# Kernel tuning notes

Measured on AMD Instinct MI355X. Metric: run time of the kernel, lower is better.

Reference implementation:

```python
import jax, jax.numpy as jnp
import numpy as np

B, S, D, H = 4, 1024, 512, 8
EPS = 1e-5


def _cx(x):
    # [..., 2] float -> complex
    return jax.lax.complex(x[..., 0], x[..., 1])


def setup_inputs() -> dict:
    key = jax.random.key(0)
    ks = jax.random.split(key, 9)
    f = lambda k, sh: jax.random.normal(k, sh, dtype=jnp.float32)
    inp = {
        "q": f(ks[0], (B, S, D, 2)),
        "k": f(ks[1], (B, S, D, 2)),
        "v": f(ks[2], (B, S, D, 2)),
        "Wq": f(ks[3], (D, D, 2)) * 0.02,
        "bq": f(ks[4], (D, 2)) * 0.02,
        "Wk": f(ks[5], (D, D, 2)) * 0.02,
        "bk": f(ks[6], (D, 2)) * 0.02,
        "Wv": f(ks[7], (D, D, 2)) * 0.02,
        "bv": f(ks[8], (D, 2)) * 0.02,
        "gamma_r": jnp.ones((D,), jnp.float32),
        "beta_r": jnp.zeros((D,), jnp.float32),
        "gamma_i": jnp.ones((D,), jnp.float32),
        "beta_i": jnp.zeros((D,), jnp.float32),
        "n_heads": H,
    }
    return inp


def _layernorm(x, g, b):
    # torch LayerNorm: biased variance, eps inside sqrt
    mu = jnp.mean(x, axis=-1, keepdims=True)
    var = jnp.mean((x - mu) ** 2, axis=-1, keepdims=True)
    return (x - mu) / jnp.sqrt(var + EPS) * g + b


def reference(q, k, v, Wq, bq, Wk, bk, Wv, bv, gamma_r, beta_r, gamma_i, beta_i, n_heads):
    qc, kc, vc = _cx(q), _cx(k), _cx(v)
    # complex linear: x @ W^T + b
    Q = jnp.einsum("bsd,ed->bse", qc, _cx(Wq)) + _cx(bq)
    K = jnp.einsum("bsd,ed->bse", kc, _cx(Wk)) + _cx(bk)
    V = jnp.einsum("bsd,ed->bse", vc, _cx(Wv)) + _cx(bv)
    b, s, d = qc.shape
    dh = d // n_heads
    Qh = Q.reshape(b, s, n_heads, dh)
    Kh = K.reshape(b, s, n_heads, dh)
    Vh = V.reshape(b, s, n_heads, dh)
    # complex scores [b,h,q,k], scaled by sqrt(dh)
    scores = jnp.einsum("bqhd,bkhd->bhqk", Qh, Kh) / jnp.sqrt(jnp.float32(dh))
    # original: softmax over view_as_real dim=-2 == key axis, real & imag independently
    attn = jax.lax.complex(jax.nn.softmax(scores.real, axis=-1),
                           jax.nn.softmax(scores.imag, axis=-1))
    # (dropout is identity in eval mode)
    out = jnp.einsum("bhqk,bkhd->bqhd", attn, Vh).reshape(b, s, d)
    out = out + qc  # residual
    out_r = _layernorm(out.real, gamma_r, beta_r)
    out_i = _layernorm(out.imag, gamma_i, beta_i)
    return jnp.stack([out_r, out_i], axis=-1)  # [B,S,D,2]
```

## Files before the change

kernel.cpp:

```cpp
#include <hip/hip_runtime.h>
#include <math.h>

#define BB  4
#define SS  1024
#define DD  512
#define HH  8
#define DHD 64
#define PL  2097152
#define WPL 262144

constexpr float LN_EPS = 1e-5f;

using half8 = __attribute__((ext_vector_type(8))) _Float16;
using f32x4 = __attribute__((ext_vector_type(4))) float;

__device__ __forceinline__ half8 negh(half8 a) {
    union { half8 h; unsigned int u[4]; } t;
    t.h = a;
    #pragma unroll
    for (int i = 0; i < 4; ++i) t.u[i] ^= 0x80008000u;
    return t.h;
}
__device__ __forceinline__ half8 ldh64(const unsigned short* p, int row, int col) {
    return *(const half8*)(p + row * 64 + (col ^ ((row & 7) << 3)));
}
__device__ __forceinline__ half8 ldh40(const unsigned short* p, int row, int col) {
    return *(const half8*)(p + row * 40 + col);
}
#define MFMA16(acc, a, b) acc = __builtin_amdgcn_mfma_f32_16x16x32_f16(a, b, acc, 0, 0, 0)

__global__ __launch_bounds__(256)
void cvt_kernel(const float2* __restrict__ s0, const float2* __restrict__ s1,
                const float2* __restrict__ s2, unsigned short* __restrict__ dst,
                int planeElems) {
    const int z = blockIdx.y;
    const float2* src = z == 0 ? s0 : (z == 1 ? s1 : s2);
    unsigned short* base = dst + (size_t)z * 2 * planeElems;
    const int idx = (blockIdx.x * 256 + threadIdx.x) * 2;
    float4 t = *(const float4*)(src + idx);
    union { _Float16 h[2]; unsigned int u; } r, i;
    r.h[0] = (_Float16)t.x; r.h[1] = (_Float16)t.z;
    i.h[0] = (_Float16)t.y; i.h[1] = (_Float16)t.w;
    ((unsigned int*)(base))[idx >> 1] = r.u;
    ((unsigned int*)(base + planeElems))[idx >> 1] = i.u;
}

__global__ __launch_bounds__(256, 5)
void proj_kernel(const unsigned short* __restrict__ XP,
                 const unsigned short* __restrict__ WP,
                 const float2* __restrict__ bq, const float2* __restrict__ bk,
                 const float2* __restrict__ bv,
                 unsigned short* __restrict__ QG, unsigned short* __restrict__ KG,
                 unsigned short* __restrict__ VG) {
    const unsigned short* XR = XP + (size_t)blockIdx.z * 2 * PL;
    const unsigned short* XI = XR + PL;
    const unsigned short* WR = WP + (size_t)blockIdx.z * 2 * WPL;
    const unsigned short* WI = WR + WPL;
    const float2* bias; unsigned short* outP;
    if (blockIdx.z == 0)      { bias = bq; outP = QG; }
    else if (blockIdx.z == 1) { bias = bk; outP = KG; }
    else                      { bias = bv; outP = VG; }
    const bool isV = (blockIdx.z == 2);

    __shared__ unsigned short Xs[2][4096];
    __shared__ unsigned short Ws[2][4096];

    const int tid  = threadIdx.x;
    const int w    = tid >> 6;
    const int lane = tid & 63;
    const int quad = lane >> 4;
    const int l15  = lane & 15;
    const int m0   = blockIdx.x * 64;
    const int h    = blockIdx.y;
    const int e0   = h * 64;

    const int r8 = tid >> 3;
    const int g8 = tid & 7;

    f32x4 Sr[4], Si[4];
    #pragma unroll
    for (int i = 0; i < 4; ++i) { Sr[i] = (f32x4)0.f; Si[i] = (f32x4)0.f; }

    for (int dc = 0; dc < DD; dc += 64) {
        if (dc) __syncthreads();
        #pragma unroll
        for (int it = 0; it < 2; ++it) {
            const int row = it * 32 + r8;
            const int off = row * 64 + ((g8 ^ (row & 7)) << 3);
            const size_t xo = (size_t)(m0 + row) * DD + dc + g8 * 8;
            const size_t wo = (size_t)(e0 + row) * DD + dc + g8 * 8;
            *(uint4*)&Xs[0][off] = *(const uint4*)(XR + xo);
            *(uint4*)&Xs[1][off] = *(const uint4*)(XI + xo);
            *(uint4*)&Ws[0][off] = *(const uint4*)(WR + wo);
            *(uint4*)&Ws[1][off] = *(const uint4*)(WI + wo);
        }
        __syncthreads();

        const int mrow = w * 16 + l15;
        #pragma unroll
        for (int kc = 0; kc < 2; ++kc) {
            const int dl = kc * 32 + quad * 8;
            half8 xr  = ldh64(Xs[0], mrow, dl);
            half8 xi  = ldh64(Xs[1], mrow, dl);
            half8 xmi = negh(xi);
            #pragma unroll
            for (int et = 0; et < 4; ++et) {
                const int er = et * 16 + l15;
                half8 wr = ldh64(Ws[0], er, dl);
                half8 wi = ldh64(Ws[1], er, dl);
                MFMA16(Sr[et], xr,  wr);
                MFMA16(Sr[et], xmi, wi);
                MFMA16(Si[et], xr,  wi);
                MFMA16(Si[et], xi,  wr);
            }
        }
    }

    #pragma unroll
    for (int et = 0; et < 4; ++et) {
        const int col = et * 16 + l15;
        float2 bb = bias[e0 + col];
        #pragma unroll
        for (int reg = 0; reg < 4; ++reg) {
            int m = m0 + w * 16 + quad * 4 + reg;
            int b = m >> 10;
            int s = m & 1023;
            int bh = b * HH + h;
            union { _Float16 h; unsigned short u; } cr, ci;
            cr.h = (_Float16)(Sr[et][reg] + bb.x);
            ci.h = (_Float16)(Si[et][reg] + bb.y);
            size_t o = isV ? ((size_t)bh * DHD + col) * SS + s
                           : ((size_t)bh * SS + s) * DHD + col;
            outP[0 * PL + o] = cr.u;
            outP[1 * PL + o] = ci.u;
        }
    }
}

__global__ __launch_bounds__(256, 3)
void attn_kernel(const unsigned short* __restrict__ QG, const unsigned short* __restrict__ KG,
                 const unsigned short* __restrict__ VG,
                 unsigned short* __restrict__ ObR, unsigned short* __restrict__ ObI) {
    __shared__ unsigned short Ks[2][2048];
    __shared__ unsigned short Vt[2][2560];
    __shared__ unsigned short Ps[2][4][640];

    const int n   = blockIdx.x;
    const int bh  = (n & 7) * 4 + (n >> 7);
    const int q0  = ((n >> 3) & 15) * 64;
    const int b   = bh >> 3;
    const int h   = bh & 7;

    const int tid  = threadIdx.x;
    const int w    = tid >> 6;
    const int lane = tid & 63;
    const int quad = lane >> 4;
    const int l15  = lane & 15;

    half8 qr[2], qi[2], qmi[2];
    #pragma unroll
    for (int kc = 0; kc < 2; ++kc) {
        size_t qb = ((size_t)bh * SS + q0 + w * 16 + l15) * DHD + kc * 32 + quad * 8;
        qr[kc]  = *(const half8*)(QG + 0 * PL + qb);
        qi[kc]  = *(const half8*)(QG + 1 * PL + qb);
        qmi[kc] = negh(qi[kc]);
    }

    f32x4 Arr[4], Ari[4], Air[4], Aii[4];
    #pragma unroll
    for (int i = 0; i < 4; ++i) { Arr[i] = (f32x4)0.f; Ari[i] = (f32x4)0.f; Air[i] = (f32x4)0.f; Aii[i] = (f32x4)0.f; }
    float lrp[4] = {0.f, 0.f, 0.f, 0.f}, lip[4] = {0.f, 0.f, 0.f, 0.f};

    unsigned short* PrW = Ps[0][w];
    unsigned short* PiW = Ps[1][w];

    const int kr = tid >> 3, sg = (tid & 7) * 8;
    const int dv = tid >> 2, sv = (tid & 3) * 8;

    for (int kt = 0; kt < SS; kt += 32) {
        if (kt) __syncthreads();
        #pragma unroll
        for (int p = 0; p < 2; ++p) {
            *(uint4*)&Ks[p][kr * 64 + (sg ^ ((kr & 7) << 3))] =
                *(const uint4*)(KG + (size_t)p * PL + ((size_t)bh * SS + kt + kr) * DHD + sg);
            *(uint4*)&Vt[p][dv * 40 + sv] =
                *(const uint4*)(VG + (size_t)p * PL + ((size_t)bh * DHD + dv) * SS + kt + sv);
        }
        __syncthreads();

        f32x4 Sr[2], Si[2];
        Sr[0] = (f32x4)0.f; Sr[1] = (f32x4)0.f; Si[0] = (f32x4)0.f; Si[1] = (f32x4)0.f;
        #pragma unroll
        for (int kc = 0; kc < 2; ++kc) {
            const int dl = kc * 32 + quad * 8;
            #pragma unroll
            for (int nt = 0; nt < 2; ++nt) {
                const int krow = nt * 16 + l15;
                half8 krF = ldh64(Ks[0], krow, dl);
                half8 kiF = ldh64(Ks[1], krow, dl);
                MFMA16(Sr[nt], qr[kc],  krF);
                MFMA16(Sr[nt], qmi[kc], kiF);
                MFMA16(Si[nt], qr[kc],  kiF);
                MFMA16(Si[nt], qi[kc],  krF);
            }
        }

        #pragma unroll
        for (int nt = 0; nt < 2; ++nt) {
            #pragma unroll
            for (int reg = 0; reg < 4; ++reg) {
                union { _Float16 h; unsigned short u; } cr, ci;
                cr.h = (_Float16)__expf(Sr[nt][reg] * 0.125f);
                ci.h = (_Float16)__expf(Si[nt][reg] * 0.125f);
                lrp[reg] += (float)cr.h;
                lip[reg] += (float)ci.h;
                int qq = quad * 4 + reg;
                int kcol = nt * 16 + l15;
                PrW[qq * 40 + kcol] = cr.u;
                PiW[qq * 40 + kcol] = ci.u;
            }
        }

        {
            const int kl = quad * 8;
            half8 prF = ldh40(PrW, l15, kl);
            half8 piF = ldh40(PiW, l15, kl);
            #pragma unroll
            for (int dt = 0; dt < 4; ++dt) {
                const int d = dt * 16 + l15;
                half8 vrF = ldh40(Vt[0], d, kl);
                half8 viF = ldh40(Vt[1], d, kl);
                MFMA16(Arr[dt], prF, vrF);
                MFMA16(Ari[dt], prF, viF);
                MFMA16(Air[dt], piF, vrF);
                MFMA16(Aii[dt], piF, viF);
            }
        }
    }

    float ir[4], ii[4];
    #pragma unroll
    for (int reg = 0; reg < 4; ++reg) {
        float a = lrp[reg], c = lip[reg];
        #pragma unroll
        for (int mk = 1; mk < 16; mk <<= 1) {
            a += __shfl_xor(a, mk);
            c += __shfl_xor(c, mk);
        }
        ir[reg] = 1.f / a;
        ii[reg] = 1.f / c;
    }
    #pragma unroll
    for (int dt = 0; dt < 4; ++dt) {
        #pragma unroll
        for (int reg = 0; reg < 4; ++reg) {
            int q   = q0 + w * 16 + quad * 4 + reg;
            int col = h * DHD + dt * 16 + l15;
            union { _Float16 h; unsigned short u; } cr, ci;
            cr.h = (_Float16)(Arr[dt][reg] * ir[reg] - Aii[dt][reg] * ii[reg]);
            ci.h = (_Float16)(Ari[dt][reg] * ir[reg] + Air[dt][reg] * ii[reg]);
            size_t o = ((size_t)b * SS + q) * DD + col;
            ObR[o] = cr.u;
            ObI[o] = ci.u;
        }
    }
}

__global__ __launch_bounds__(256)
void ln_kernel(const unsigned short* __restrict__ OrP, const unsigned short* __restrict__ OiP,
               const float2* __restrict__ Qin,
               const float* __restrict__ gr, const float* __restrict__ br,
               const float* __restrict__ gi, const float* __restrict__ bi,
               float2* __restrict__ out) {
    const int row = blockIdx.x;
    const int tid = threadIdx.x;
    const size_t base = (size_t)row * DD;
    const int e0 = 2 * tid, e1 = 2 * tid + 1;

    union { unsigned int u; _Float16 h[2]; } tr, ti;
    tr.u = *(const unsigned int*)(OrP + base + e0);
    ti.u = *(const unsigned int*)(OiP + base + e0);
    float2 r0 = Qin[base + e0];
    float2 r1 = Qin[base + e1];
    float xr0 = (float)tr.h[0] + r0.x;
    float xr1 = (float)tr.h[1] + r1.x;
    float xi0 = (float)ti.h[0] + r0.y;
    float xi1 = (float)ti.h[1] + r1.y;

    float sr = xr0 + xr1;
    float si = xi0 + xi1;
    float qr = xr0 * xr0 + xr1 * xr1;
    float qi = xi0 * xi0 + xi1 * xi1;
    #pragma unroll
    for (int off = 32; off > 0; off >>= 1) {
        sr += __shfl_down(sr, off);
        si += __shfl_down(si, off);
        qr += __shfl_down(qr, off);
        qi += __shfl_down(qi, off);
    }
    __shared__ float red[4][4];
    __shared__ float stat[4];
    int lane = tid & 63, wid = tid >> 6;
    if (lane == 0) { red[wid][0] = sr; red[wid][1] = si; red[wid][2] = qr; red[wid][3] = qi; }
    __syncthreads();
    if (tid == 0) {
        sr = red[0][0] + red[1][0] + red[2][0] + red[3][0];
        si = red[0][1] + red[1][1] + red[2][1] + red[3][1];
        qr = red[0][2] + red[1][2] + red[2][2] + red[3][2];
        qi = red[0][3] + red[1][3] + red[2][3] + red[3][3];
        float mur = sr * (1.f / DD), mui = si * (1.f / DD);
        float vr = qr * (1.f / DD) - mur * mur;
        float vi = qi * (1.f / DD) - mui * mui;
        stat[0] = mur; stat[1] = mui;
        stat[2] = rsqrtf(vr + LN_EPS); stat[3] = rsqrtf(vi + LN_EPS);
    }
    __syncthreads();
    float mur = stat[0], mui = stat[1], rsr = stat[2], rsi = stat[3];
    out[base + e0] = make_float2((xr0 - mur) * rsr * gr[e0] + br[e0],
                                 (xi0 - mui) * rsi * gi[e0] + bi[e0]);
    out[base + e1] = make_float2((xr1 - mur) * rsr * gr[e1] + br[e1],
                                 (xi1 - mui) * rsi * gi[e1] + bi[e1]);
}

extern "C" void kernel_launch(void* const* d_in, const int* in_sizes, int n_in,
                              void* d_out, int out_size, void* d_ws, size_t ws_size,
                              hipStream_t stream) {
    const float2* q  = (const float2*)d_in[0];
    const float2* k  = (const float2*)d_in[1];
    const float2* v  = (const float2*)d_in[2];
    const float2* Wq = (const float2*)d_in[3];
    const float2* bq = (const float2*)d_in[4];
    const float2* Wk = (const float2*)d_in[5];
    const float2* bk = (const float2*)d_in[6];
    const float2* Wv = (const float2*)d_in[7];
    const float2* bv = (const float2*)d_in[8];
    const float*  gr = (const float*)d_in[9];
    const float*  br = (const float*)d_in[10];
    const float*  gi = (const float*)d_in[11];
    const float*  bi = (const float*)d_in[12];

    unsigned short* XP  = (unsigned short*)d_ws;
    unsigned short* WP  = XP + (size_t)6 * PL;
    unsigned short* QG  = WP + (size_t)6 * WPL;
    unsigned short* KG  = QG + (size_t)2 * PL;
    unsigned short* VG  = KG + (size_t)2 * PL;
    unsigned short* ObR = VG + (size_t)2 * PL;
    unsigned short* ObI = ObR + (size_t)PL;

    cvt_kernel<<<dim3(4096, 3), 256, 0, stream>>>(q, k, v, XP, PL);
    cvt_kernel<<<dim3(512, 3), 256, 0, stream>>>(Wq, Wk, Wv, WP, WPL);
    proj_kernel<<<dim3(64, 8, 3), 256, 0, stream>>>(XP, WP, bq, bk, bv, QG, KG, VG);
    attn_kernel<<<dim3(512), 256, 0, stream>>>(QG, KG, VG, ObR, ObI);
    ln_kernel<<<dim3(BB * SS), 256, 0, stream>>>(ObR, ObI, q, gr, br, gi, bi, (float2*)d_out);
}
```

Before: 225.6 us.

## Restructure attention kernel into 2x2 warp tiling with 64-key tiles

```diff
diff --git a/kernel.cpp b/kernel.cpp
--- a/kernel.cpp
+++ b/kernel.cpp
@@ -11,6 +11,7 @@
 
 constexpr float LN_EPS = 1e-5f;
 
+using half4 = __attribute__((ext_vector_type(4))) _Float16;
 using half8 = __attribute__((ext_vector_type(8))) _Float16;
 using f32x4 = __attribute__((ext_vector_type(4))) float;
 
@@ -23,9 +24,6 @@
 }
 __device__ __forceinline__ half8 ldh64(const unsigned short* p, int row, int col) {
     return *(const half8*)(p + row * 64 + (col ^ ((row & 7) << 3)));
-}
-__device__ __forceinline__ half8 ldh40(const unsigned short* p, int row, int col) {
-    return *(const half8*)(p + row * 40 + col);
 }
 #define MFMA16(acc, a, b) acc = __builtin_amdgcn_mfma_f32_16x16x32_f16(a, b, acc, 0, 0, 0)
 
@@ -137,13 +135,15 @@
     }
 }
 
-__global__ __launch_bounds__(256, 3)
+#define AWID 72
+__global__ __launch_bounds__(256, 2)
 void attn_kernel(const unsigned short* __restrict__ QG, const unsigned short* __restrict__ KG,
                  const unsigned short* __restrict__ VG,
                  unsigned short* __restrict__ ObR, unsigned short* __restrict__ ObI) {
-    __shared__ unsigned short Ks[2][2048];
-    __shared__ unsigned short Vt[2][2560];
-    __shared__ unsigned short Ps[2][4][640];
+    __shared__ unsigned short Ks[2][64 * AWID];
+    __shared__ unsigned short Vt[2][64 * AWID];
+    __shared__ unsigned short Ps[2][64 * AWID];
+    __shared__ float lbuf[2][2][64];
 
     const int n   = blockIdx.x;
     const int bh  = (n & 7) * 4 + (n >> 7);
@@ -156,114 +156,147 @@
     const int lane = tid & 63;
     const int quad = lane >> 4;
     const int l15  = lane & 15;
-
-    half8 qr[2], qi[2], qmi[2];
-    #pragma unroll
-    for (int kc = 0; kc < 2; ++kc) {
-        size_t qb = ((size_t)bh * SS + q0 + w * 16 + l15) * DHD + kc * 32 + quad * 8;
-        qr[kc]  = *(const half8*)(QG + 0 * PL + qb);
-        qi[kc]  = *(const half8*)(QG + 1 * PL + qb);
-        qmi[kc] = negh(qi[kc]);
-    }
-
-    f32x4 Arr[4], Ari[4], Air[4], Aii[4];
-    #pragma unroll
-    for (int i = 0; i < 4; ++i) { Arr[i] = (f32x4)0.f; Ari[i] = (f32x4)0.f; Air[i] = (f32x4)0.f; Aii[i] = (f32x4)0.f; }
-    float lrp[4] = {0.f, 0.f, 0.f, 0.f}, lip[4] = {0.f, 0.f, 0.f, 0.f};
-
-    unsigned short* PrW = Ps[0][w];
-    unsigned short* PiW = Ps[1][w];
-
-    const int kr = tid >> 3, sg = (tid & 7) * 8;
-    const int dv = tid >> 2, sv = (tid & 3) * 8;
-
-    for (int kt = 0; kt < SS; kt += 32) {
-        if (kt) __syncthreads();
+    const int sw   = w & 1;
+    const int tw   = w >> 1;
+
+    half8 qfr[2][2], qfi[2][2], qfmi[2][2];
+    #pragma unroll
+    for (int qt = 0; qt < 2; ++qt)
+        #pragma unroll
+        for (int kc = 0; kc < 2; ++kc) {
+            size_t qa = ((size_t)bh * SS + q0 + sw * 32 + qt * 16 + l15) * DHD + kc * 32 + quad * 8;
+            qfr[qt][kc]  = *(const half8*)(QG + qa);
+            qfi[qt][kc]  = *(const half8*)(QG + PL + qa);
+            qfmi[qt][kc] = negh(qfi[qt][kc]);
+        }
+
+    f32x4 acc[2][2][4];
+    #pragma unroll
+    for (int qt = 0; qt < 2; ++qt)
+        #pragma unroll
+        for (int dt = 0; dt < 2; ++dt)
+            #pragma unroll
+            for (int p = 0; p < 4; ++p) acc[qt][dt][p] = (f32x4)0.f;
+    float lacc[2][2] = {{0.f, 0.f}, {0.f, 0.f}};
+
+    const int srow = tid >> 3;
+    const int sg   = (tid & 7) * 8;
+
+    for (int kt = 0; kt < SS; kt += 64) {
+        __syncthreads();
+        #pragma unroll
+        for (int p = 0; p < 2; ++p)
+            #pragma unroll
+            for (int it = 0; it < 2; ++it) {
+                const int r = it * 32 + srow;
+                *(uint4*)&Ks[p][r * AWID + sg] =
+                    *(const uint4*)(KG + (size_t)p * PL + ((size_t)bh * SS + kt + r) * DHD + sg);
+                *(uint4*)&Vt[p][r * AWID + sg] =
+                    *(const uint4*)(VG + (size_t)p * PL + ((size_t)bh * DHD + r) * SS + kt + sg);
+            }
+        __syncthreads();
+
+        f32x4 Sr[2][2], Si[2][2];
+        #pragma unroll
+        for (int a = 0; a < 2; ++a)
+            #pragma unroll
+            for (int c = 0; c < 2; ++c) { Sr[a][c] = (f32x4)0.f; Si[a][c] = (f32x4)0.f; }
+        #pragma unroll
+        for (int kc = 0; kc < 2; ++kc) {
+            #pragma unroll
+            for (int kt2 = 0; kt2 < 2; ++kt2) {
+                const int krow = tw * 32 + kt2 * 16 + l15;
+                half8 akr = *(const half8*)&Ks[0][krow * AWID + kc * 32 + quad * 8];
+                half8 aki = *(const half8*)&Ks[1][krow * AWID + kc * 32 + quad * 8];
+                #pragma unroll
+                for (int qt = 0; qt < 2; ++qt) {
+                    MFMA16(Sr[kt2][qt], akr, qfr[qt][kc]);
+                    MFMA16(Sr[kt2][qt], aki, qfmi[qt][kc]);
+                    MFMA16(Si[kt2][qt], aki, qfr[qt][kc]);
+                    MFMA16(Si[kt2][qt], akr, qfi[qt][kc]);
+                }
+            }
+        }
+
+        #pragma unroll
+        for (int kt2 = 0; kt2 < 2; ++kt2)
+            #pragma unroll
+            for (int qt = 0; qt < 2; ++qt) {
+                half4 pr, pi;
+                float sr_ = 0.f, si_ = 0.f;
+                #pragma unroll
+                for (int reg = 0; reg < 4; ++reg) {
+                    float er = __expf(Sr[kt2][qt][reg] * 0.125f);
+                    float ei = __expf(Si[kt2][qt][reg] * 0.125f);
+                    pr[reg] = (_Float16)er;
+                    pi[reg] = (_Float16)ei;
+                    sr_ += (float)pr[reg];
+                    si_ += (float)pi[reg];
+                }
+                lacc[qt][0] += sr_;
+                lacc[qt][1] += si_;
+                const int qrow = sw * 32 + qt * 16 + l15;
+                const int kcol = tw * 32 + kt2 * 16 + quad * 4;
+                *(half4*)&Ps[0][qrow * AWID + kcol] = pr;
+                *(half4*)&Ps[1][qrow * AWID + kcol] = pi;
+            }
+        __syncthreads();
+
+        #pragma unroll
+        for (int kc = 0; kc < 2; ++kc) {
+            half8 ap[2][2];
+            #pragma unroll
+            for (int qt = 0; qt < 2; ++qt) {
+                const int qrow = sw * 32 + qt * 16 + l15;
+                ap[qt][0] = *(const half8*)&Ps[0][qrow * AWID + kc * 32 + quad * 8];
+                ap[qt][1] = *(const half8*)&Ps[1][qrow * AWID + kc * 32 + quad * 8];
+            }
+            #pragma unroll
+            for (int dt = 0; dt < 2; ++dt) {
+                const int drow = tw * 32 + dt * 16 + l15;
+                half8 bvr = *(const half8*)&Vt[0][drow * AWID + kc * 32 + quad * 8];
+                half8 bvi = *(const half8*)&Vt[1][drow * AWID + kc * 32 + quad * 8];
+                #pragma unroll
+                for (int qt = 0; qt < 2; ++qt) {
+                    MFMA16(acc[qt][dt][0], ap[qt][0], bvr);
+                    MFMA16(acc[qt][dt][1], ap[qt][0], bvi);
+                    MFMA16(acc[qt][dt][2], ap[qt][1], bvr);
+                    MFMA16(acc[qt][dt][3], ap[qt][1], bvi);
+                }
+            }
+        }
+    }
+
+    __syncthreads();
+    #pragma unroll
+    for (int qt = 0; qt < 2; ++qt)
         #pragma unroll
         for (int p = 0; p < 2; ++p) {
-            *(uint4*)&Ks[p][kr * 64 + (sg ^ ((kr & 7) << 3))] =
-                *(const uint4*)(KG + (size_t)p * PL + ((size_t)bh * SS + kt + kr) * DHD + sg);
-            *(uint4*)&Vt[p][dv * 40 + sv] =
-                *(const uint4*)(VG + (size_t)p * PL + ((size_t)bh * DHD + dv) * SS + kt + sv);
-        }
-        __syncthreads();
-
-        f32x4 Sr[2], Si[2];
-        Sr[0] = (f32x4)0.f; Sr[1] = (f32x4)0.f; Si[0] = (f32x4)0.f; Si[1] = (f32x4)0.f;
-        #pragma unroll
-        for (int kc = 0; kc < 2; ++kc) {
-            const int dl = kc * 32 + quad * 8;
-            #pragma unroll
-            for (int nt = 0; nt < 2; ++nt) {
-                const int krow = nt * 16 + l15;
-                half8 krF = ldh64(Ks[0], krow, dl);
-                half8 kiF = ldh64(Ks[1], krow, dl);
-                MFMA16(Sr[nt], qr[kc],  krF);
-                MFMA16(Sr[nt], qmi[kc], kiF);
-                MFMA16(Si[nt], qr[kc],  kiF);
-                MFMA16(Si[nt], qi[kc],  krF);
-            }
-        }
-
-        #pragma unroll
-        for (int nt = 0; nt < 2; ++nt) {
-            #pragma unroll
-            for (int reg = 0; reg < 4; ++reg) {
+            float v = lacc[qt][p];
+            v += __shfl_xor(v, 16);
+            v += __shfl_xor(v, 32);
+            if (lane < 16) lbuf[p][tw][sw * 32 + qt * 16 + lane] = v;
+        }
+    __syncthreads();
+
+    #pragma unroll
+    for (int qt = 0; qt < 2; ++qt)
+        #pragma unroll
+        for (int reg = 0; reg < 4; ++reg) {
+            const int qloc = sw * 32 + qt * 16 + quad * 4 + reg;
+            const float ir = 1.f / (lbuf[0][0][qloc] + lbuf[0][1][qloc]);
+            const float ii = 1.f / (lbuf[1][0][qloc] + lbuf[1][1][qloc]);
+            #pragma unroll
+            for (int dt = 0; dt < 2; ++dt) {
+                const int d = tw * 32 + dt * 16 + l15;
                 union { _Float16 h; unsigned short u; } cr, ci;
-                cr.h = (_Float16)__expf(Sr[nt][reg] * 0.125f);
-                ci.h = (_Float16)__expf(Si[nt][reg] * 0.125f);
-                lrp[reg] += (float)cr.h;
-                lip[reg] += (float)ci.h;
-                int qq = quad * 4 + reg;
-                int kcol = nt * 16 + l15;
-                PrW[qq * 40 + kcol] = cr.u;
-                PiW[qq * 40 + kcol] = ci.u;
-            }
-        }
-
-        {
-            const int kl = quad * 8;
-            half8 prF = ldh40(PrW, l15, kl);
-            half8 piF = ldh40(PiW, l15, kl);
-            #pragma unroll
-            for (int dt = 0; dt < 4; ++dt) {
-                const int d = dt * 16 + l15;
-                half8 vrF = ldh40(Vt[0], d, kl);
-                half8 viF = ldh40(Vt[1], d, kl);
-                MFMA16(Arr[dt], prF, vrF);
-                MFMA16(Ari[dt], prF, viF);
-                MFMA16(Air[dt], piF, vrF);
-                MFMA16(Aii[dt], piF, viF);
-            }
-        }
-    }
-
-    float ir[4], ii[4];
-    #pragma unroll
-    for (int reg = 0; reg < 4; ++reg) {
-        float a = lrp[reg], c = lip[reg];
-        #pragma unroll
-        for (int mk = 1; mk < 16; mk <<= 1) {
-            a += __shfl_xor(a, mk);
-            c += __shfl_xor(c, mk);
-        }
-        ir[reg] = 1.f / a;
-        ii[reg] = 1.f / c;
-    }
-    #pragma unroll
-    for (int dt = 0; dt < 4; ++dt) {
-        #pragma unroll
-        for (int reg = 0; reg < 4; ++reg) {
-            int q   = q0 + w * 16 + quad * 4 + reg;
-            int col = h * DHD + dt * 16 + l15;
-            union { _Float16 h; unsigned short u; } cr, ci;
-            cr.h = (_Float16)(Arr[dt][reg] * ir[reg] - Aii[dt][reg] * ii[reg]);
-            ci.h = (_Float16)(Ari[dt][reg] * ir[reg] + Air[dt][reg] * ii[reg]);
-            size_t o = ((size_t)b * SS + q) * DD + col;
-            ObR[o] = cr.u;
-            ObI[o] = ci.u;
-        }
-    }
+                cr.h = (_Float16)(acc[qt][dt][0][reg] * ir - acc[qt][dt][3][reg] * ii);
+                ci.h = (_Float16)(acc[qt][dt][1][reg] * ir + acc[qt][dt][2][reg] * ii);
+                size_t o = ((size_t)b * SS + q0 + qloc) * DD + h * DHD + d;
+                ObR[o] = cr.u;
+                ObI[o] = ci.u;
+            }
+        }
 }
 
 __global__ __launch_bounds__(256)
```

Result: no change. 224.7 us (-0.4%).
